# Performance work log

Measured on AMD Instinct MI355X. Metric: run time of the kernel, lower is better.

The kernel has to match this reference:

```python
import jax, jax.numpy as jnp
import numpy as np

V, E, ENC, D, A = 10000, 512, 2048, 512, 512  # vocab, embed, encoder_dim, decoder_dim, attention_dim
B, L, T = 64, 49, 20


def setup_inputs() -> dict:
    key = jax.random.key(0)
    ks = jax.random.split(key, 20)
    s = lambda k, shape, fan: jax.random.normal(k, shape, jnp.float32) / np.sqrt(fan)
    return {
        "encoder_out": jax.random.normal(ks[0], (B, L, ENC), jnp.float32),
        "captions": jax.random.randint(ks[1], (B, T), 0, V),
        "emb_table": s(ks[2], (V, E), E),
        "W_enc_att": s(ks[3], (ENC, A), ENC), "b_enc_att": jnp.zeros((A,), jnp.float32),
        "W_dec_att": s(ks[4], (D, A), D), "b_dec_att": jnp.zeros((A,), jnp.float32),
        "w_full": s(ks[5], (A,), A), "b_full": jnp.zeros((), jnp.float32),
        "W_ih": s(ks[6], (4 * D, E + ENC), E + ENC), "b_ih": jnp.zeros((4 * D,), jnp.float32),
        "W_hh": s(ks[7], (4 * D, D), D), "b_hh": jnp.zeros((4 * D,), jnp.float32),
        "W_init_h": s(ks[8], (ENC, D), ENC), "b_init_h": jnp.zeros((D,), jnp.float32),
        "W_init_c": s(ks[9], (ENC, D), ENC), "b_init_c": jnp.zeros((D,), jnp.float32),
        "W_out": s(ks[10], (D, V), D), "b_out": jnp.zeros((V,), jnp.float32),
    }


def _decoder(encoder_out, captions, emb_table, W_enc_att, b_enc_att, W_dec_att,
             b_dec_att, w_full, b_full, W_ih, b_ih, W_hh, b_hh,
             W_init_h, b_init_h, W_init_c, b_init_c, W_out, b_out):
    # init hidden/cell from mean encoder features
    mean_enc = encoder_out.mean(axis=1)                      # (B, ENC)
    h = mean_enc @ W_init_h + b_init_h                        # (B, D)
    c = mean_enc @ W_init_c + b_init_c
    # precompute encoder projection for additive attention (shared across steps)
    enc_proj = jnp.einsum('ble,ea->bla', encoder_out, W_enc_att) + b_enc_att  # (B, L, A)
    embeddings = emb_table[captions]                          # (B, T, E)
    emb_seq = jnp.swapaxes(embeddings, 0, 1)                  # (T, B, E)
    Dh = h.shape[-1]

    def step(carry, emb_t):
        h, c = carry
        # additive attention over L=49 locations
        dec_proj = h @ W_dec_att + b_dec_att                  # (B, A)
        att = jax.nn.relu(enc_proj + dec_proj[:, None, :])    # (B, L, A)
        scores = jnp.einsum('bla,a->bl', att, w_full) + b_full
        alpha = jax.nn.softmax(scores, axis=-1)               # (B, L)
        context = jnp.einsum('bl,ble->be', alpha, encoder_out)  # (B, ENC)
        # LSTMCell (PyTorch gate order: i, f, g, o)
        x = jnp.concatenate([emb_t, context], axis=1)         # (B, E+ENC)
        gates = x @ W_ih.T + b_ih + h @ W_hh.T + b_hh         # (B, 4D)
        i, f, g, o = jnp.split(gates, 4, axis=1)
        i, f, o = jax.nn.sigmoid(i), jax.nn.sigmoid(f), jax.nn.sigmoid(o)
        g = jnp.tanh(g)
        c_new = f * c + i * g
        h_new = o * jnp.tanh(c_new)
        # dropout is identity in eval mode
        logits_t = h_new @ W_out + b_out                      # (B, V)
        return (h_new, c_new), (logits_t, alpha)

    (_, _), (logits, alphas) = jax.lax.scan(step, (h, c), emb_seq)
    logits = jnp.swapaxes(logits, 0, 1)                       # (B, T, V)
    alphas = jnp.swapaxes(alphas, 0, 1)                       # (B, T, L)
    return logits, alphas


def reference(encoder_out, captions, emb_table, W_enc_att, b_enc_att, W_dec_att,
              b_dec_att, w_full, b_full, W_ih, b_ih, W_hh, b_hh,
              W_init_h, b_init_h, W_init_c, b_init_c, W_out, b_out):
    return _decoder(encoder_out, captions, emb_table, W_enc_att, b_enc_att,
                    W_dec_att, b_dec_att, w_full, b_full, W_ih, b_ih, W_hh, b_hh,
                    W_init_h, b_init_h, W_init_c, b_init_c, W_out, b_out)
```

## Files before the change

### kernel.cpp

```cpp
#include <hip/hip_runtime.h>
#include <hip/hip_bf16.h>

constexpr int NV   = 10000;
constexpr int NE   = 512;
constexpr int NENC = 2048;
constexpr int ND   = 512;
constexpr int NA   = 512;
constexpr int NB   = 64;
constexpr int NL   = 49;
constexpr int NT   = 20;
constexpr int KX   = NE + NENC + ND;
constexpr int KIH  = NE + NENC;

typedef short bfrag __attribute__((ext_vector_type(8)));
typedef float f32x4 __attribute__((ext_vector_type(4)));

__device__ __forceinline__ float us2f(unsigned short u) {
    union { unsigned int i; float f; } x; x.i = (unsigned int)u << 16; return x.f;
}
__device__ __forceinline__ unsigned short f2us(float f) {
    union { float f_; unsigned int u; } x; x.f_ = f;
    unsigned int r = (x.u + 0x7fffu + ((x.u >> 16) & 1u)) >> 16;
    return (unsigned short)r;
}

__launch_bounds__(256)
__global__ void k_mean(const float* __restrict__ enc, unsigned short* __restrict__ meanbf)
{
    const int b = blockIdx.x;
    const int e = blockIdx.y * 256 + threadIdx.x;
    const float* p = enc + (size_t)b * NL * NENC + e;
    float s = 0.f;
    #pragma unroll 7
    for (int l = 0; l < NL; ++l) s += p[(size_t)l * NENC];
    meanbf[(size_t)b * NENC + e] = f2us(s * (1.0f / NL));
}

__launch_bounds__(256)
__global__ void k_init_mfma(const unsigned short* __restrict__ meanbf,
                            const unsigned short* __restrict__ WicT,
                            const float* __restrict__ bh, const float* __restrict__ bc,
                            unsigned short* __restrict__ hbf, float* __restrict__ c)
{
    const int wave = threadIdx.x >> 6, lane = threadIdx.x & 63;
    const int m0 = wave * 16, n0 = blockIdx.x * 16;
    const int r = lane & 15, quad = lane >> 4;
    const unsigned short* ap = meanbf + (size_t)(m0 + r) * NENC + quad * 8;
    const unsigned short* bp = WicT   + (size_t)(n0 + r) * NENC + quad * 8;
    f32x4 acc = {0.f, 0.f, 0.f, 0.f};
    #pragma unroll 8
    for (int k = 0; k < NENC; k += 32) {
        bfrag a = *(const bfrag*)(ap + k);
        bfrag b = *(const bfrag*)(bp + k);
        acc = __builtin_amdgcn_mfma_f32_16x16x32_bf16(a, b, acc, 0, 0, 0);
    }
    const int n = n0 + r;
    const bool isC = n >= ND;
    const float bv = isC ? bc[n - ND] : bh[n];
    #pragma unroll
    for (int i = 0; i < 4; ++i) {
        int m = m0 + quad * 4 + i;
        float v = acc[i] + bv;
        if (isC) c[(size_t)m * ND + (n - ND)] = v;
        else     hbf[(size_t)m * ND + n] = f2us(v);
    }
}

__launch_bounds__(256)
__global__ void k_cvt(const float* __restrict__ src, unsigned short* __restrict__ dst, int n)
{
    int i = (blockIdx.x * 256 + threadIdx.x) * 4;
    if (i < n) {
        float4 v = *(const float4*)(src + i);
        dst[i + 0] = f2us(v.x); dst[i + 1] = f2us(v.y);
        dst[i + 2] = f2us(v.z); dst[i + 3] = f2us(v.w);
    }
}

__launch_bounds__(256)
__global__ void k_transpose(const float* __restrict__ src, unsigned short* __restrict__ dst,
                            int K, int N)
{
    __shared__ float t[32][33];
    const int nb = blockIdx.x * 32, kb = blockIdx.y * 32;
    const int tx = threadIdx.x & 31, ty = threadIdx.x >> 5;
    #pragma unroll
    for (int i = ty; i < 32; i += 8) {
        int n = nb + tx;
        t[i][tx] = (n < N) ? src[(size_t)(kb + i) * N + n] : 0.f;
    }
    __syncthreads();
    #pragma unroll
    for (int i = ty; i < 32; i += 8) {
        int n = nb + i;
        if (n < N) dst[(size_t)n * K + kb + tx] = f2us(t[tx][i]);
    }
}

__launch_bounds__(256)
__global__ void k_encproj_mfma(const unsigned short* __restrict__ encb,
                               const unsigned short* __restrict__ WeaT,
                               const float* __restrict__ bias,
                               unsigned short* __restrict__ epb)
{
    const int j = (blockIdx.x & 7) * 49 + (blockIdx.x >> 3);
    const int ng = j & 7;
    const int mg = j >> 3;
    const int wave = threadIdx.x >> 6, lane = threadIdx.x & 63;
    const int wm = wave >> 1, wn = wave & 1;
    const int m0 = mg * 64 + wm * 32;
    const int n0 = ng * 64 + wn * 32;
    const int r = lane & 15, quad = lane >> 4;
    const unsigned short* ap0 = encb + (size_t)(m0 + r) * NENC + quad * 8;
    const unsigned short* ap1 = ap0 + (size_t)16 * NENC;
    const unsigned short* bp0 = WeaT + (size_t)(n0 + r) * NENC + quad * 8;
    const unsigned short* bp1 = bp0 + (size_t)16 * NENC;
    f32x4 acc00 = {0.f,0.f,0.f,0.f}, acc01 = {0.f,0.f,0.f,0.f};
    f32x4 acc10 = {0.f,0.f,0.f,0.f}, acc11 = {0.f,0.f,0.f,0.f};
    #pragma unroll 4
    for (int k = 0; k < NENC; k += 32) {
        bfrag a0 = *(const bfrag*)(ap0 + k);
        bfrag a1 = *(const bfrag*)(ap1 + k);
        bfrag b0 = *(const bfrag*)(bp0 + k);
        bfrag b1 = *(const bfrag*)(bp1 + k);
        acc00 = __builtin_amdgcn_mfma_f32_16x16x32_bf16(a0, b0, acc00, 0, 0, 0);
        acc01 = __builtin_amdgcn_mfma_f32_16x16x32_bf16(a0, b1, acc01, 0, 0, 0);
        acc10 = __builtin_amdgcn_mfma_f32_16x16x32_bf16(a1, b0, acc10, 0, 0, 0);
        acc11 = __builtin_amdgcn_mfma_f32_16x16x32_bf16(a1, b1, acc11, 0, 0, 0);
    }
    const float bv0 = bias[n0 + r], bv1 = bias[n0 + 16 + r];
    #pragma unroll
    for (int i = 0; i < 4; ++i) {
        int ma = m0 + quad * 4 + i, mb = ma + 16;
        epb[(size_t)ma * NA + n0 + r]      = f2us(acc00[i] + bv0);
        epb[(size_t)ma * NA + n0 + 16 + r] = f2us(acc01[i] + bv1);
        epb[(size_t)mb * NA + n0 + r]      = f2us(acc10[i] + bv0);
        epb[(size_t)mb * NA + n0 + 16 + r] = f2us(acc11[i] + bv1);
    }
}

__device__ __forceinline__ void logits_tasks(int t, int lo, int hi,
    int worker, int nworkers, int wave, int lane,
    const unsigned short* hbf, const unsigned short* WoutT,
    const float* bout, float* out)
{
    const int slot = wave >> 2, w4 = wave & 3;
    const int r = lane & 15, quad = lane >> 4;
    const int m0 = w4 * 16;
    for (int task = lo + worker * 2 + slot; task < hi; task += nworkers * 2) {
        const int n0 = task * 16;
        const unsigned short* ap = hbf + (size_t)(m0 + r) * ND + quad * 8;
        const unsigned short* bp = WoutT + (size_t)(n0 + r) * ND + quad * 8;
        f32x4 acc = {0.f, 0.f, 0.f, 0.f};
        #pragma unroll
        for (int k = 0; k < ND; k += 32) {
            bfrag a = *(const bfrag*)(ap + k);
            bfrag b = *(const bfrag*)(bp + k);
            acc = __builtin_amdgcn_mfma_f32_16x16x32_bf16(a, b, acc, 0, 0, 0);
        }
        const float bv = bout[n0 + r];
        #pragma unroll
        for (int i = 0; i < 4; ++i) {
            int m = m0 + quad * 4 + i;
            out[((size_t)m * NT + t) * NV + n0 + r] = acc[i] + bv;
        }
    }
}

__device__ __forceinline__ void att_body(int t, int b, int tid,
    const unsigned short* hcur, const float* dpg, const unsigned short* epb,
    const unsigned short* encb, const float* wf, const float* bfs,
    const float* embt, const int* caps, unsigned short* x, float* alpha_out,
    float* dp , float* al )
{
    for (int d = tid; d < ND; d += 512)
        x[(size_t)b * KX + NE + NENC + d] = hcur[(size_t)b * ND + d];
    for (int a = tid; a < NA; a += 512)
        dp[a] = dpg[(size_t)b * NA + a];
    const int tok = caps[b * NT + t];
    for (int j = tid; j < NE; j += 512)
        x[(size_t)b * KX + j] = f2us(embt[(size_t)tok * NE + j]);
    __syncthreads();

    const int wave = tid >> 6, lane = tid & 63;
    const float bfull = bfs[0];
    for (int l = wave; l < NL; l += 8) {
        const unsigned short* ep = epb + ((size_t)b * NL + l) * NA;
        float s = 0.f;
        #pragma unroll
        for (int a = lane; a < NA; a += 64) {
            float v = us2f(ep[a]) + dp[a];
            v = v > 0.f ? v : 0.f;
            s = fmaf(v, wf[a], s);
        }
        #pragma unroll
        for (int off = 32; off > 0; off >>= 1) s += __shfl_down(s, off, 64);
        if (lane == 0) al[l] = s + bfull;
    }
    __syncthreads();

    if (tid < 64) {
        float v = (tid < NL) ? al[tid] : -1e30f;
        float m = v;
        #pragma unroll
        for (int off = 32; off > 0; off >>= 1) m = fmaxf(m, __shfl_xor(m, off, 64));
        float e = (tid < NL) ? expf(v - m) : 0.f;
        float s = e;
        #pragma unroll
        for (int off = 32; off > 0; off >>= 1) s += __shfl_xor(s, off, 64);
        float a = e / s;
        if (tid < NL) {
            al[tid] = a;
            alpha_out[((size_t)b * NT + t) * NL + tid] = a;
        }
    }
    __syncthreads();

    {
        const int e = tid * 4;
        const unsigned short* p = encb + (size_t)b * NL * NENC + e;
        float s0 = 0.f, s1 = 0.f, s2 = 0.f, s3 = 0.f;
        #pragma unroll 7
        for (int l = 0; l < NL; ++l) {
            ushort4 v = *(const ushort4*)(p + (size_t)l * NENC);
            float a = al[l];
            s0 = fmaf(a, us2f(v.x), s0);
            s1 = fmaf(a, us2f(v.y), s1);
            s2 = fmaf(a, us2f(v.z), s2);
            s3 = fmaf(a, us2f(v.w), s3);
        }
        unsigned short* xo = x + (size_t)b * KX + NE + e;
        xo[0] = f2us(s0); xo[1] = f2us(s1); xo[2] = f2us(s2); xo[3] = f2us(s3);
    }
}

__launch_bounds__(512)
__global__ void k_att_logits(int t,
                             const unsigned short* __restrict__ hcur,
                             const float* __restrict__ dpg,
                             const unsigned short* __restrict__ epb,
                             const unsigned short* __restrict__ encb,
                             const float* __restrict__ wf,
                             const float* __restrict__ bfs,
                             const float* __restrict__ embt,
                             const int* __restrict__ captions,
                             unsigned short* __restrict__ x,
                             float* __restrict__ alpha_out,
                             const unsigned short* __restrict__ WoutT,
                             const float* __restrict__ bout,
                             float* __restrict__ out)
{
    __shared__ float smem[576];
    const int bid = blockIdx.x, tid = threadIdx.x;
    if (bid < 64) {
        att_body(t, bid, tid, hcur, dpg, epb, encb, wf, bfs,
                 embt, captions, x, alpha_out, smem, smem + 512);
    } else if (t > 0) {
        logits_tasks(t - 1, 0, 384, bid - 64, 192, tid >> 6, tid & 63,
                     hcur, WoutT, bout, out);
    }
}

__launch_bounds__(512)
__global__ void k_gates_lstm(int t,
                             const unsigned short* __restrict__ x,
                             const unsigned short* __restrict__ Wihb,
                             const unsigned short* __restrict__ Whhb,
                             const float* __restrict__ bih, const float* __restrict__ bhh,
                             unsigned short* __restrict__ hnxt, float* __restrict__ c,
                             const unsigned short* __restrict__ hcur,
                             const unsigned short* __restrict__ WoutT,
                             const float* __restrict__ bout,
                             float* __restrict__ out)
{
    __shared__ float part[7 * 4 * 16 * 16];
    const int bid = blockIdx.x;
    const int wave = threadIdx.x >> 6, lane = threadIdx.x & 63;
    if (bid >= 128) {
        if (t > 0)
            logits_tasks(t - 1, 384, 625, bid - 128, 121, wave, lane,
                         hcur, WoutT, bout, out);
        return;
    }
    const int ng = (bid & 7) * 4 + ((bid >> 3) & 3);
    const int mt = bid >> 5;
    const int m0 = mt * 16, n0 = ng * 16;
    const int r = lane & 15, quad = lane >> 4;
    const int k0 = wave * (KX / 8), k1 = k0 + (KX / 8);

    const unsigned short* ap = x + (size_t)(m0 + r) * KX + quad * 8;
    const unsigned short* bpih[4];
    const unsigned short* bphh[4];
    #pragma unroll
    for (int g = 0; g < 4; ++g) {
        bpih[g] = Wihb + (size_t)(g * ND + n0 + r) * KIH + quad * 8;
        bphh[g] = Whhb + (size_t)(g * ND + n0 + r) * ND + quad * 8;
    }
    f32x4 acc[4] = {{0.f,0.f,0.f,0.f},{0.f,0.f,0.f,0.f},
                    {0.f,0.f,0.f,0.f},{0.f,0.f,0.f,0.f}};

    const int kiA = (k1 < KIH) ? k1 : KIH;
    #pragma unroll 4
    for (int k = k0; k < kiA; k += 32) {
        bfrag a = *(const bfrag*)(ap + k);
        #pragma unroll
        for (int g = 0; g < 4; ++g) {
            bfrag b = *(const bfrag*)(bpih[g] + k);
            acc[g] = __builtin_amdgcn_mfma_f32_16x16x32_bf16(a, b, acc[g], 0, 0, 0);
        }
    }
    const int kiB = (k0 > KIH) ? k0 : KIH;
    #pragma unroll 4
    for (int k = kiB; k < k1; k += 32) {
        bfrag a = *(const bfrag*)(ap + k);
        #pragma unroll
        for (int g = 0; g < 4; ++g) {
            bfrag b = *(const bfrag*)(bphh[g] + (k - KIH));
            acc[g] = __builtin_amdgcn_mfma_f32_16x16x32_bf16(a, b, acc[g], 0, 0, 0);
        }
    }

    if (wave > 0) {
        #pragma unroll
        for (int g = 0; g < 4; ++g)
            #pragma unroll
            for (int i = 0; i < 4; ++i)
                part[(((wave - 1) * 4 + g) * 16 + quad * 4 + i) * 16 + r] = acc[g][i];
    }
    __syncthreads();
    if (wave == 0) {
        #pragma unroll
        for (int g = 0; g < 4; ++g)
            #pragma unroll
            for (int i = 0; i < 4; ++i) {
                float v = acc[g][i];
                #pragma unroll
                for (int w = 0; w < 7; ++w)
                    v += part[((w * 4 + g) * 16 + quad * 4 + i) * 16 + r];
                acc[g][i] = v;
            }
        const int d = n0 + r;
        const float b0 = bih[d]        + bhh[d];
        const float b1 = bih[d + 512]  + bhh[d + 512];
        const float b2 = bih[d + 1024] + bhh[d + 1024];
        const float b3 = bih[d + 1536] + bhh[d + 1536];
        #pragma unroll
        for (int i = 0; i < 4; ++i) {
            const int m = m0 + quad * 4 + i;
            float gi = acc[0][i] + b0;
            float gf = acc[1][i] + b1;
            float gg = acc[2][i] + b2;
            float go = acc[3][i] + b3;
            float ig = 1.f / (1.f + expf(-gi));
            float fg = 1.f / (1.f + expf(-gf));
            float g  = tanhf(gg);
            float og = 1.f / (1.f + expf(-go));
            float cn = fg * c[(size_t)m * ND + d] + ig * g;
            float hn = og * tanhf(cn);
            c[(size_t)m * ND + d] = cn;
            hnxt[(size_t)m * ND + d] = f2us(hn);
        }
    }
}

__launch_bounds__(512)
__global__ void k_decproj(const unsigned short* __restrict__ hbf,
                          const unsigned short* __restrict__ WdaT,
                          const float* __restrict__ bda, float* __restrict__ dp)
{
    const int wave = threadIdx.x >> 6, lane = threadIdx.x & 63;
    const int slot = wave >> 2, w4 = wave & 3;
    const int tile = blockIdx.x * 2 + slot;
    const int n0 = tile * 16, m0 = w4 * 16;
    const int r = lane & 15, quad = lane >> 4;
    const unsigned short* ap = hbf + (size_t)(m0 + r) * ND + quad * 8;
    const unsigned short* bp = WdaT + (size_t)(n0 + r) * ND + quad * 8;
    f32x4 acc = {0.f, 0.f, 0.f, 0.f};
    #pragma unroll
    for (int k = 0; k < ND; k += 32) {
        bfrag a = *(const bfrag*)(ap + k);
        bfrag b = *(const bfrag*)(bp + k);
        acc = __builtin_amdgcn_mfma_f32_16x16x32_bf16(a, b, acc, 0, 0, 0);
    }
    const float bv = bda[n0 + r];
    #pragma unroll
    for (int i = 0; i < 4; ++i) {
        int m = m0 + quad * 4 + i;
        dp[(size_t)m * NA + n0 + r] = acc[i] + bv;
    }
}

__launch_bounds__(512)
__global__ void k_logits_fin(int t,
                             const unsigned short* __restrict__ hbf,
                             const unsigned short* __restrict__ WoutT,
                             const float* __restrict__ bout,
                             float* __restrict__ out)
{
    logits_tasks(t, 0, 625, blockIdx.x, 313, threadIdx.x >> 6, threadIdx.x & 63,
                 hbf, WoutT, bout, out);
}

extern "C" void kernel_launch(void* const* d_in, const int* in_sizes, int n_in,
                              void* d_out, int out_size, void* d_ws, size_t ws_size,
                              hipStream_t stream) {
    const float* enc  = (const float*)d_in[0];
    const int*   caps = (const int*)d_in[1];
    const float* embt = (const float*)d_in[2];
    const float* Wea  = (const float*)d_in[3];
    const float* bea  = (const float*)d_in[4];
    const float* Wda  = (const float*)d_in[5];
    const float* bda  = (const float*)d_in[6];
    const float* wf   = (const float*)d_in[7];
    const float* bfs  = (const float*)d_in[8];
    const float* Wih  = (const float*)d_in[9];
    const float* bih  = (const float*)d_in[10];
    const float* Whh  = (const float*)d_in[11];
    const float* bhh  = (const float*)d_in[12];
    const float* Wh0  = (const float*)d_in[13];
    const float* bh0  = (const float*)d_in[14];
    const float* Wc0  = (const float*)d_in[15];
    const float* bc0  = (const float*)d_in[16];
    const float* Wout = (const float*)d_in[17];
    const float* bout = (const float*)d_in[18];

    float* out = (float*)d_out;
    float* alpha_out = out + (size_t)NB * NT * NV;

    char* w = (char*)d_ws;
    float* c     = (float*)w;                 w += (size_t)NB * ND * 4;
    float* dp    = (float*)w;                 w += (size_t)NB * NA * 4;
    unsigned short* meanbf = (unsigned short*)w; w += (size_t)NB * NENC * 2;
    unsigned short* hb    = (unsigned short*)w; w += (size_t)2 * NB * ND * 2;
    unsigned short* x     = (unsigned short*)w; w += (size_t)NB * KX * 2;
    unsigned short* epb   = (unsigned short*)w; w += (size_t)NB * NL * NA * 2;
    unsigned short* encb  = (unsigned short*)w; w += (size_t)NB * NL * NENC * 2;
    unsigned short* Wihb  = (unsigned short*)w; w += (size_t)4 * ND * KIH * 2;
    unsigned short* Whhb  = (unsigned short*)w; w += (size_t)4 * ND * ND * 2;
    unsigned short* WeaT  = (unsigned short*)w; w += (size_t)NA * NENC * 2;
    unsigned short* WdaT  = (unsigned short*)w; w += (size_t)NA * ND * 2;
    unsigned short* WoutT = (unsigned short*)w; w += (size_t)NV * ND * 2;
    unsigned short* WicT  = (unsigned short*)w; w += (size_t)2 * ND * NENC * 2;

    hipLaunchKernelGGL(k_mean, dim3(NB, NENC / 256), dim3(256), 0, stream, enc, meanbf);
    hipLaunchKernelGGL(k_transpose, dim3(ND / 32, NENC / 32), dim3(256), 0, stream,
                       Wh0, WicT, NENC, ND);
    hipLaunchKernelGGL(k_transpose, dim3(ND / 32, NENC / 32), dim3(256), 0, stream,
                       Wc0, WicT + (size_t)ND * NENC, NENC, ND);
    hipLaunchKernelGGL(k_init_mfma, dim3(2 * ND / 16), dim3(256), 0, stream,
                       meanbf, WicT, bh0, bc0, hb, c);
    {
        int n = NB * NL * NENC;
        hipLaunchKernelGGL(k_cvt, dim3(n / 4 / 256), dim3(256), 0, stream, enc, encb, n);
    }
    {
        int n = 4 * ND * KIH;
        hipLaunchKernelGGL(k_cvt, dim3(n / 4 / 256), dim3(256), 0, stream, Wih, Wihb, n);
    }
    {
        int n = 4 * ND * ND;
        hipLaunchKernelGGL(k_cvt, dim3(n / 4 / 256), dim3(256), 0, stream, Whh, Whhb, n);
    }
    hipLaunchKernelGGL(k_transpose, dim3(NA / 32, NENC / 32), dim3(256), 0, stream,
                       Wea, WeaT, NENC, NA);
    hipLaunchKernelGGL(k_transpose, dim3(NA / 32, ND / 32), dim3(256), 0, stream,
                       Wda, WdaT, ND, NA);
    hipLaunchKernelGGL(k_transpose, dim3((NV + 31) / 32, ND / 32), dim3(256), 0, stream,
                       Wout, WoutT, ND, NV);
    hipLaunchKernelGGL(k_encproj_mfma, dim3((NB * NL / 64) * (NA / 64)), dim3(256), 0, stream,
                       encb, WeaT, bea, epb);
    hipLaunchKernelGGL(k_decproj, dim3(16), dim3(512), 0, stream, hb, WdaT, bda, dp);

    for (int t = 0; t < NT; ++t) {
        unsigned short* hcur = hb + (size_t)(t & 1) * NB * ND;
        unsigned short* hnxt = hb + (size_t)((t + 1) & 1) * NB * ND;
        hipLaunchKernelGGL(k_att_logits, dim3(256), dim3(512), 0, stream,
                           t, hcur, dp, epb, encb, wf, bfs, embt, caps,
                           x, alpha_out, WoutT, bout, out);
        hipLaunchKernelGGL(k_gates_lstm, dim3(249), dim3(512), 0, stream,
                           t, x, Wihb, Whhb, bih, bhh, hnxt, c,
                           hcur, WoutT, bout, out);
        if (t + 1 < NT)
            hipLaunchKernelGGL(k_decproj, dim3(16), dim3(512), 0, stream,
                               hnxt, WdaT, bda, dp);
    }
    hipLaunchKernelGGL(k_logits_fin, dim3(313), dim3(512), 0, stream,
                       NT - 1, hb + (size_t)(NT & 1) * NB * ND, WoutT, bout, out);
}
```

Before: 1.038 ms.

## Fuse decoder-projection into attention, merge prep kernels, retile encproj and gate reduction

The per-step decoder attention projection is folded into the attention block: each batch block computes its own row of h·W_dec_att with MFMA, which removes a separate kernel launch and a global dp buffer from every timestep. The three fp32-to-bf16 conversion launches are merged into one kernel, and the five weight transposes are merged into another, to cut launch overhead during setup. The encoder-projection GEMM is retiled to 784 smaller blocks for more parallelism. The LSTM gate reduction now has all 8 waves write partials and 256 threads do the reduction and activation, replacing the single-wave epilogue. In exchange, the fused decoder projection wastes most of each MFMA, since it feeds a single batch row through a 16-row tile, and this work sits on the attention critical path.

```diff
diff --git a/kernel.cpp b/kernel.cpp
--- a/kernel.cpp
+++ b/kernel.cpp
@@ -67,22 +67,39 @@
 }
 
 __launch_bounds__(256)
-__global__ void k_cvt(const float* __restrict__ src, unsigned short* __restrict__ dst, int n)
-{
-    int i = (blockIdx.x * 256 + threadIdx.x) * 4;
-    if (i < n) {
-        float4 v = *(const float4*)(src + i);
-        dst[i + 0] = f2us(v.x); dst[i + 1] = f2us(v.y);
-        dst[i + 2] = f2us(v.z); dst[i + 3] = f2us(v.w);
-    }
+__global__ void k_cvt3(const float* __restrict__ s0, unsigned short* __restrict__ d0,
+                       const float* __restrict__ s1, unsigned short* __restrict__ d1,
+                       const float* __restrict__ s2, unsigned short* __restrict__ d2)
+{
+    int bid = blockIdx.x;
+    const float* src; unsigned short* dst;
+    if (bid < 6272)       { src = s0; dst = d0; }
+    else if (bid < 11392) { src = s1; dst = d1; bid -= 6272; }
+    else                  { src = s2; dst = d2; bid -= 11392; }
+    const int i = bid * 1024 + threadIdx.x * 4;
+    float4 v = *(const float4*)(src + i);
+    dst[i + 0] = f2us(v.x); dst[i + 1] = f2us(v.y);
+    dst[i + 2] = f2us(v.z); dst[i + 3] = f2us(v.w);
 }
 
 __launch_bounds__(256)
-__global__ void k_transpose(const float* __restrict__ src, unsigned short* __restrict__ dst,
-                            int K, int N)
+__global__ void k_transpose_all(const float* __restrict__ Wh0, const float* __restrict__ Wc0,
+                                const float* __restrict__ Wea, const float* __restrict__ Wda,
+                                const float* __restrict__ Wout,
+                                unsigned short* __restrict__ WicT,
+                                unsigned short* __restrict__ WeaT,
+                                unsigned short* __restrict__ WdaT,
+                                unsigned short* __restrict__ WoutT)
 {
     __shared__ float t[32][33];
-    const int nb = blockIdx.x * 32, kb = blockIdx.y * 32;
+    int bid = blockIdx.x;
+    const float* src; unsigned short* dst; int K, N, nCols;
+    if (bid < 1024)      { src = Wh0;  dst = WicT;                       K = NENC; N = ND; nCols = 16; }
+    else if (bid < 2048) { src = Wc0;  dst = WicT + (size_t)ND * NENC;   K = NENC; N = ND; nCols = 16; bid -= 1024; }
+    else if (bid < 3072) { src = Wea;  dst = WeaT;                       K = NENC; N = NA; nCols = 16; bid -= 2048; }
+    else if (bid < 3328) { src = Wda;  dst = WdaT;                       K = ND;   N = NA; nCols = 16; bid -= 3072; }
+    else                 { src = Wout; dst = WoutT;                      K = ND;   N = NV; nCols = 313; bid -= 3328; }
+    const int nb = (bid % nCols) * 32, kb = (bid / nCols) * 32;
     const int tx = threadIdx.x & 31, ty = threadIdx.x >> 5;
     #pragma unroll
     for (int i = ty; i < 32; i += 8) {
@@ -103,39 +120,32 @@
                                const float* __restrict__ bias,
                                unsigned short* __restrict__ epb)
 {
-    const int j = (blockIdx.x & 7) * 49 + (blockIdx.x >> 3);
-    const int ng = j & 7;
-    const int mg = j >> 3;
+    const int j = (blockIdx.x & 7) * 98 + (blockIdx.x >> 3);
+    const int ngr = j & 15;
+    const int mg  = j >> 4;
     const int wave = threadIdx.x >> 6, lane = threadIdx.x & 63;
-    const int wm = wave >> 1, wn = wave & 1;
+    const int wm = wave & 1, wn = wave >> 1;
     const int m0 = mg * 64 + wm * 32;
-    const int n0 = ng * 64 + wn * 32;
+    const int n0 = ngr * 32 + wn * 16;
     const int r = lane & 15, quad = lane >> 4;
     const unsigned short* ap0 = encb + (size_t)(m0 + r) * NENC + quad * 8;
     const unsigned short* ap1 = ap0 + (size_t)16 * NENC;
     const unsigned short* bp0 = WeaT + (size_t)(n0 + r) * NENC + quad * 8;
-    const unsigned short* bp1 = bp0 + (size_t)16 * NENC;
-    f32x4 acc00 = {0.f,0.f,0.f,0.f}, acc01 = {0.f,0.f,0.f,0.f};
-    f32x4 acc10 = {0.f,0.f,0.f,0.f}, acc11 = {0.f,0.f,0.f,0.f};
-    #pragma unroll 4
+    f32x4 acc0 = {0.f,0.f,0.f,0.f}, acc1 = {0.f,0.f,0.f,0.f};
+    #pragma unroll 8
     for (int k = 0; k < NENC; k += 32) {
         bfrag a0 = *(const bfrag*)(ap0 + k);
         bfrag a1 = *(const bfrag*)(ap1 + k);
         bfrag b0 = *(const bfrag*)(bp0 + k);
-        bfrag b1 = *(const bfrag*)(bp1 + k);
-        acc00 = __builtin_amdgcn_mfma_f32_16x16x32_bf16(a0, b0, acc00, 0, 0, 0);
-        acc01 = __builtin_amdgcn_mfma_f32_16x16x32_bf16(a0, b1, acc01, 0, 0, 0);
-        acc10 = __builtin_amdgcn_mfma_f32_16x16x32_bf16(a1, b0, acc10, 0, 0, 0);
-        acc11 = __builtin_amdgcn_mfma_f32_16x16x32_bf16(a1, b1, acc11, 0, 0, 0);
-    }
-    const float bv0 = bias[n0 + r], bv1 = bias[n0 + 16 + r];
+        acc0 = __builtin_amdgcn_mfma_f32_16x16x32_bf16(a0, b0, acc0, 0, 0, 0);
+        acc1 = __builtin_amdgcn_mfma_f32_16x16x32_bf16(a1, b0, acc1, 0, 0, 0);
+    }
+    const float bv = bias[n0 + r];
     #pragma unroll
     for (int i = 0; i < 4; ++i) {
-        int ma = m0 + quad * 4 + i, mb = ma + 16;
-        epb[(size_t)ma * NA + n0 + r]      = f2us(acc00[i] + bv0);
-        epb[(size_t)ma * NA + n0 + 16 + r] = f2us(acc01[i] + bv1);
-        epb[(size_t)mb * NA + n0 + r]      = f2us(acc10[i] + bv0);
-        epb[(size_t)mb * NA + n0 + 16 + r] = f2us(acc11[i] + bv1);
+        int ma = m0 + quad * 4 + i;
+        epb[(size_t)ma * NA + n0 + r]        = f2us(acc0[i] + bv);
+        epb[(size_t)(ma + 16) * NA + n0 + r] = f2us(acc1[i] + bv);
     }
 }
 
@@ -168,21 +178,37 @@
 }
 
 __device__ __forceinline__ void att_body(int t, int b, int tid,
-    const unsigned short* hcur, const float* dpg, const unsigned short* epb,
-    const unsigned short* encb, const float* wf, const float* bfs,
+    const unsigned short* hcur, const unsigned short* epb,
+    const unsigned short* encb, const unsigned short* WdaT,
+    const float* bda, const float* wf, const float* bfs,
     const float* embt, const int* caps, unsigned short* x, float* alpha_out,
     float* dp , float* al )
 {
-    for (int d = tid; d < ND; d += 512)
-        x[(size_t)b * KX + NE + NENC + d] = hcur[(size_t)b * ND + d];
-    for (int a = tid; a < NA; a += 512)
-        dp[a] = dpg[(size_t)b * NA + a];
+    const int wave = tid >> 6, lane = tid & 63;
+    const int r = lane & 15, quad = lane >> 4;
+
+    x[(size_t)b * KX + NE + NENC + tid] = hcur[(size_t)b * ND + tid];
     const int tok = caps[b * NT + t];
-    for (int j = tid; j < NE; j += 512)
-        x[(size_t)b * KX + j] = f2us(embt[(size_t)tok * NE + j]);
+    x[(size_t)b * KX + tid] = f2us(embt[(size_t)tok * NE + tid]);
+
+    {
+        const unsigned short* hb_row = hcur + (size_t)b * ND;
+        #pragma unroll
+        for (int jj = 0; jj < 4; ++jj) {
+            const int n0 = (wave * 4 + jj) * 16;
+            const unsigned short* bp = WdaT + (size_t)(n0 + r) * ND + quad * 8;
+            f32x4 acc = {0.f, 0.f, 0.f, 0.f};
+            #pragma unroll
+            for (int k = 0; k < ND; k += 32) {
+                bfrag a = *(const bfrag*)(hb_row + k + quad * 8);
+                bfrag bb = *(const bfrag*)(bp + k);
+                acc = __builtin_amdgcn_mfma_f32_16x16x32_bf16(a, bb, acc, 0, 0, 0);
+            }
+            if (quad == 0) dp[n0 + r] = acc[0] + bda[n0 + r];
+        }
+    }
     __syncthreads();
 
-    const int wave = tid >> 6, lane = tid & 63;
     const float bfull = bfs[0];
     for (int l = wave; l < NL; l += 8) {
         const unsigned short* ep = epb + ((size_t)b * NL + l) * NA;
@@ -237,9 +263,10 @@
 __launch_bounds__(512)
 __global__ void k_att_logits(int t,
                              const unsigned short* __restrict__ hcur,
-                             const float* __restrict__ dpg,
                              const unsigned short* __restrict__ epb,
                              const unsigned short* __restrict__ encb,
+                             const unsigned short* __restrict__ WdaT,
+                             const float* __restrict__ bda,
                              const float* __restrict__ wf,
                              const float* __restrict__ bfs,
                              const float* __restrict__ embt,
@@ -253,7 +280,7 @@
     __shared__ float smem[576];
     const int bid = blockIdx.x, tid = threadIdx.x;
     if (bid < 64) {
-        att_body(t, bid, tid, hcur, dpg, epb, encb, wf, bfs,
+        att_body(t, bid, tid, hcur, epb, encb, WdaT, bda, wf, bfs,
                  embt, captions, x, alpha_out, smem, smem + 512);
     } else if (t > 0) {
         logits_tasks(t - 1, 0, 384, bid - 64, 192, tid >> 6, tid & 63,
@@ -273,7 +300,7 @@
                              const float* __restrict__ bout,
                              float* __restrict__ out)
 {
-    __shared__ float part[7 * 4 * 16 * 16];
+    __shared__ float part[8 * 4 * 16 * 16];
     const int bid = blockIdx.x;
     const int wave = threadIdx.x >> 6, lane = threadIdx.x & 63;
     if (bid >= 128) {
@@ -320,73 +347,38 @@
         }
     }
 
-    if (wave > 0) {
-        #pragma unroll
-        for (int g = 0; g < 4; ++g)
+    #pragma unroll
+    for (int g = 0; g < 4; ++g)
+        #pragma unroll
+        for (int i = 0; i < 4; ++i)
+            part[((wave * 4 + g) * 16 + quad * 4 + i) * 16 + r] = acc[g][i];
+    __syncthreads();
+
+    if (threadIdx.x < 256) {
+        const int row = threadIdx.x >> 4, col = threadIdx.x & 15;
+        float gs[4];
+        #pragma unroll
+        for (int g = 0; g < 4; ++g) {
+            float v = 0.f;
             #pragma unroll
-            for (int i = 0; i < 4; ++i)
-                part[(((wave - 1) * 4 + g) * 16 + quad * 4 + i) * 16 + r] = acc[g][i];
-    }
-    __syncthreads();
-    if (wave == 0) {
-        #pragma unroll
-        for (int g = 0; g < 4; ++g)
-            #pragma unroll
-            for (int i = 0; i < 4; ++i) {
-                float v = acc[g][i];
-                #pragma unroll
-                for (int w = 0; w < 7; ++w)
-                    v += part[((w * 4 + g) * 16 + quad * 4 + i) * 16 + r];
-                acc[g][i] = v;
-            }
-        const int d = n0 + r;
-        const float b0 = bih[d]        + bhh[d];
-        const float b1 = bih[d + 512]  + bhh[d + 512];
-        const float b2 = bih[d + 1024] + bhh[d + 1024];
-        const float b3 = bih[d + 1536] + bhh[d + 1536];
-        #pragma unroll
-        for (int i = 0; i < 4; ++i) {
-            const int m = m0 + quad * 4 + i;
-            float gi = acc[0][i] + b0;
-            float gf = acc[1][i] + b1;
-            float gg = acc[2][i] + b2;
-            float go = acc[3][i] + b3;
-            float ig = 1.f / (1.f + expf(-gi));
-            float fg = 1.f / (1.f + expf(-gf));
-            float g  = tanhf(gg);
-            float og = 1.f / (1.f + expf(-go));
-            float cn = fg * c[(size_t)m * ND + d] + ig * g;
-            float hn = og * tanhf(cn);
-            c[(size_t)m * ND + d] = cn;
-            hnxt[(size_t)m * ND + d] = f2us(hn);
-        }
-    }
-}
-
-__launch_bounds__(512)
-__global__ void k_decproj(const unsigned short* __restrict__ hbf,
-                          const unsigned short* __restrict__ WdaT,
-                          const float* __restrict__ bda, float* __restrict__ dp)
-{
-    const int wave = threadIdx.x >> 6, lane = threadIdx.x & 63;
-    const int slot = wave >> 2, w4 = wave & 3;
-    const int tile = blockIdx.x * 2 + slot;
-    const int n0 = tile * 16, m0 = w4 * 16;
-    const int r = lane & 15, quad = lane >> 4;
-    const unsigned short* ap = hbf + (size_t)(m0 + r) * ND + quad * 8;
-    const unsigned short* bp = WdaT + (size_t)(n0 + r) * ND + quad * 8;
-    f32x4 acc = {0.f, 0.f, 0.f, 0.f};
-    #pragma unroll
-    for (int k = 0; k < ND; k += 32) {
-        bfrag a = *(const bfrag*)(ap + k);
-        bfrag b = *(const bfrag*)(bp + k);
-        acc = __builtin_amdgcn_mfma_f32_16x16x32_bf16(a, b, acc, 0, 0, 0);
-    }
-    const float bv = bda[n0 + r];
-    #pragma unroll
-    for (int i = 0; i < 4; ++i) {
-        int m = m0 + quad * 4 + i;
-        dp[(size_t)m * NA + n0 + r] = acc[i] + bv;
+            for (int w = 0; w < 8; ++w)
+                v += part[((w * 4 + g) * 16 + row) * 16 + col];
+            gs[g] = v;
+        }
+        const int d = n0 + col;
+        const int m = m0 + row;
+        float gi = gs[0] + bih[d]        + bhh[d];
+        float gf = gs[1] + bih[d + 512]  + bhh[d + 512];
+        float gg = gs[2] + bih[d + 1024] + bhh[d + 1024];
+        float go = gs[3] + bih[d + 1536] + bhh[d + 1536];
+        float ig = 1.f / (1.f + expf(-gi));
+        float fg = 1.f / (1.f + expf(-gf));
+        float g  = tanhf(gg);
+        float og = 1.f / (1.f + expf(-go));
+        float cn = fg * c[(size_t)m * ND + d] + ig * g;
+        float hn = og * tanhf(cn);
+        c[(size_t)m * ND + d] = cn;
+        hnxt[(size_t)m * ND + d] = f2us(hn);
     }
 }
 
@@ -429,7 +421,6 @@
 
     char* w = (char*)d_ws;
     float* c     = (float*)w;                 w += (size_t)NB * ND * 4;
-    float* dp    = (float*)w;                 w += (size_t)NB * NA * 4;
     unsigned short* meanbf = (unsigned short*)w; w += (size_t)NB * NENC * 2;
     unsigned short* hb    = (unsigned short*)w; w += (size_t)2 * NB * ND * 2;
     unsigned short* x     = (unsigned short*)w; w += (size_t)NB * KX * 2;
@@ -443,46 +434,24 @@
     unsigned short* WicT  = (unsigned short*)w; w += (size_t)2 * ND * NENC * 2;
 
     hipLaunchKernelGGL(k_mean, dim3(NB, NENC / 256), dim3(256), 0, stream, enc, meanbf);
-    hipLaunchKernelGGL(k_transpose, dim3(ND / 32, NENC / 32), dim3(256), 0, stream,
-                       Wh0, WicT, NENC, ND);
-    hipLaunchKernelGGL(k_transpose, dim3(ND / 32, NENC / 32), dim3(256), 0, stream,
-                       Wc0, WicT + (size_t)ND * NENC, NENC, ND);
+    hipLaunchKernelGGL(k_cvt3, dim3(12416), dim3(256), 0, stream,
+                       enc, encb, Wih, Wihb, Whh, Whhb);
+    hipLaunchKernelGGL(k_transpose_all, dim3(8336), dim3(256), 0, stream,
+                       Wh0, Wc0, Wea, Wda, Wout, WicT, WeaT, WdaT, WoutT);
     hipLaunchKernelGGL(k_init_mfma, dim3(2 * ND / 16), dim3(256), 0, stream,
                        meanbf, WicT, bh0, bc0, hb, c);
-    {
-        int n = NB * NL * NENC;
-        hipLaunchKernelGGL(k_cvt, dim3(n / 4 / 256), dim3(256), 0, stream, enc, encb, n);
-    }
-    {
-        int n = 4 * ND * KIH;
-        hipLaunchKernelGGL(k_cvt, dim3(n / 4 / 256), dim3(256), 0, stream, Wih, Wihb, n);
-    }
-    {
-        int n = 4 * ND * ND;
-        hipLaunchKernelGGL(k_cvt, dim3(n / 4 / 256), dim3(256), 0, stream, Whh, Whhb, n);
-    }
-    hipLaunchKernelGGL(k_transpose, dim3(NA / 32, NENC / 32), dim3(256), 0, stream,
-                       Wea, WeaT, NENC, NA);
-    hipLaunchKernelGGL(k_transpose, dim3(NA / 32, ND / 32), dim3(256), 0, stream,
-                       Wda, WdaT, ND, NA);
-    hipLaunchKernelGGL(k_transpose, dim3((NV + 31) / 32, ND / 32), dim3(256), 0, stream,
-                       Wout, WoutT, ND, NV);
-    hipLaunchKernelGGL(k_encproj_mfma, dim3((NB * NL / 64) * (NA / 64)), dim3(256), 0, stream,
+    hipLaunchKernelGGL(k_encproj_mfma, dim3(784), dim3(256), 0, stream,
                        encb, WeaT, bea, epb);
-    hipLaunchKernelGGL(k_decproj, dim3(16), dim3(512), 0, stream, hb, WdaT, bda, dp);
 
     for (int t = 0; t < NT; ++t) {
         unsigned short* hcur = hb + (size_t)(t & 1) * NB * ND;
         unsigned short* hnxt = hb + (size_t)((t + 1) & 1) * NB * ND;
         hipLaunchKernelGGL(k_att_logits, dim3(256), dim3(512), 0, stream,
-                           t, hcur, dp, epb, encb, wf, bfs, embt, caps,
+                           t, hcur, epb, encb, WdaT, bda, wf, bfs, embt, caps,
                            x, alpha_out, WoutT, bout, out);
         hipLaunchKernelGGL(k_gates_lstm, dim3(249), dim3(512), 0, stream,
                            t, x, Wihb, Whhb, bih, bhh, hnxt, c,
                            hcur, WoutT, bout, out);
-        if (t + 1 < NT)
-            hipLaunchKernelGGL(k_decproj, dim3(16), dim3(512), 0, stream,
-                               hnxt, WdaT, bda, dp);
     }
     hipLaunchKernelGGL(k_logits_fin, dim3(313), dim3(512), 0, stream,
                        NT - 1, hb + (size_t)(NT & 1) * NB * ND, WoutT, bout, out);
```

New measurement: 1.153 ms. 1.11x slower.
